# Kernel tuning notes

Hardware: AMD Instinct MI355X
Metric: run time of the kernel (lower is better)

The kernel has to match this reference:

```python
import jax, jax.numpy as jnp
import numpy as np

B, S, D, H = 8, 2048, 1024, 64


def setup_inputs() -> dict:
    key = jax.random.key(0)
    ks = jax.random.split(key, 9)
    s = 0.02
    return {
        "x": jax.random.normal(ks[0], (B, S, D), jnp.float32),
        "Wq": jax.random.normal(ks[1], (H, D), jnp.float32) * s,
        "bq": jnp.zeros((H,), jnp.float32),
        "Wk": jax.random.normal(ks[2], (H, D), jnp.float32) * s,
        "bk": jnp.zeros((H,), jnp.float32),
        "Wv": jax.random.normal(ks[3], (H, D), jnp.float32) * s,
        "bv": jnp.zeros((H,), jnp.float32),
        "Wo": jax.random.normal(ks[4], (H, H), jnp.float32) * s,
        "bo": jnp.zeros((H,), jnp.float32),
    }


def reference(x, Wq, bq, Wk, bk, Wv, bv, Wo, bo):
    # Linear layers: y = x @ W.T + b (torch nn.Linear convention)
    q = jnp.einsum("bsd,hd->bsh", x, Wq) + bq  # [B,S,H]
    k = jnp.einsum("bsd,hd->bsh", x, Wk) + bk
    v = jnp.einsum("bsd,hd->bsh", x, Wv) + bv
    scale = jnp.float32(H) ** 0.5
    scores = jnp.einsum("bsh,bth->bst", q, k) / scale  # [B,S,S]
    causal = jnp.tril(jnp.ones((S, S), bool))
    scores = jnp.where(causal, scores, -jnp.inf)
    attn = jax.nn.softmax(scores, axis=-1)
    out = jnp.einsum("bst,bth->bsh", attn, v)  # [B,S,H]
    out = jnp.einsum("bsh,gh->bsg", out, Wo) + bo  # output proj [H,H]
    return out
```

## Files before the change

### kernel.cpp

```cpp
#include <hip/hip_runtime.h>
#include <hip/hip_bf16.h>

#define NB 8
#define NS 2048
#define ND 1024
#define NH 64
#define NM (NB*NS)

typedef __attribute__((ext_vector_type(8))) short short8;
typedef __attribute__((ext_vector_type(4))) short short4v;
typedef __attribute__((ext_vector_type(4))) float f32x4;
typedef __attribute__((ext_vector_type(4))) float f4;
typedef __attribute__((ext_vector_type(2))) unsigned int uint2v;

#define QSCALE (0.125f * 1.44269504088896340736f)

__device__ __forceinline__ unsigned short f2bf(float f) {
    union { __hip_bfloat16 h; unsigned short u; } cv;
    cv.h = __float2bfloat16(f);
    return cv.u;
}

__device__ __forceinline__ void barrier_nd() {
    asm volatile("s_waitcnt lgkmcnt(0)" ::: "memory");
    __builtin_amdgcn_s_barrier();
    asm volatile("" ::: "memory");
}

__global__ __launch_bounds__(256) void convw_kernel(
    const float* __restrict__ Wq, const float* __restrict__ bq,
    const float* __restrict__ Wk, const float* __restrict__ bk,
    const float* __restrict__ Wv, const float* __restrict__ bv,
    const float* __restrict__ Wo,
    unsigned short* __restrict__ Wb, unsigned short* __restrict__ Wob,
    float* __restrict__ biasb)
{
    const int row = blockIdx.x;
    const int t = threadIdx.x;
    if (row < 192) {
        const float* W = row < 64 ? Wq : (row < 128 ? Wk : Wv);
        const float sc = row < 64 ? QSCALE : 1.0f;
        f4 v = *(const f4*)&W[(size_t)(row & 63) * ND + t * 4];
        short4v o;
#pragma unroll
        for (int j = 0; j < 4; ++j) o[j] = (short)f2bf(v[j] * sc);
        *(short4v*)&Wb[(size_t)row * ND + t * 4] = o;
        if (row == 0 && t < 192) {
            const float* bsrc = t < 64 ? bq : (t < 128 ? bk : bv);
            biasb[t] = bsrc[t & 63] * (t < 64 ? QSCALE : 1.0f);
        }
    } else if (t < 16) {
        f4 v = *(const f4*)&Wo[(size_t)(row - 192) * 64 + t * 4];
        short4v o;
#pragma unroll
        for (int j = 0; j < 4; ++j) o[j] = (short)f2bf(v[j]);
        *(short4v*)&Wob[(size_t)(row - 192) * 64 + t * 4] = o;
    }
}

__global__ __launch_bounds__(512, 2) void qkv_kernel(
    const float* __restrict__ x, const unsigned short* __restrict__ Wb,
    const float* __restrict__ biasb,
    unsigned short* __restrict__ q, unsigned short* __restrict__ k,
    unsigned short* __restrict__ vT)
{
    __shared__ unsigned short As[2][64 * 64];
    __shared__ unsigned short Bs[2][192 * 64];

    const int t = threadIdx.x;
    const int lane = t & 63, g = lane >> 4, li = lane & 15;
    const int w = t >> 6, rg = w >> 2, cg = w & 3;
    const int m0 = blockIdx.x * 64;
    const int arow = t >> 3, ach = t & 7;

    f32x4 acc[2][3];
#pragma unroll
    for (int a = 0; a < 2; ++a)
#pragma unroll
        for (int nf = 0; nf < 3; ++nf) acc[a][nf] = (f32x4)0.f;

    f4 xa[3][2]; short8 wr[3][3];

#define QKV_LOAD(KS, SL)                                                          \
    {                                                                             \
        const float* p_ = &x[(size_t)(m0 + arow) * ND + (KS) * 64 + ach * 8];     \
        xa[SL][0] = *(const f4*)p_; xa[SL][1] = *(const f4*)(p_ + 4);             \
        wr[SL][0] = *(const short8*)&Wb[(size_t)(t >> 3) * ND + (KS) * 64 + (t & 7) * 8];                  \
        wr[SL][1] = *(const short8*)&Wb[(size_t)((t + 512) >> 3) * ND + (KS) * 64 + ((t + 512) & 7) * 8];  \
        wr[SL][2] = *(const short8*)&Wb[(size_t)((t + 1024) >> 3) * ND + (KS) * 64 + ((t + 1024) & 7) * 8];\
    }

#define QKV_COMMIT(SL, BUF)                                                       \
    {                                                                             \
        short8 av_;                                                               \
        for (int j_ = 0; j_ < 4; ++j_) {                                          \
            av_[j_] = (short)f2bf(xa[SL][0][j_]);                                 \
            av_[j_ + 4] = (short)f2bf(xa[SL][1][j_]);                             \
        }                                                                         \
        *(short8*)&As[BUF][arow * 64 + ((ach ^ (arow & 7)) << 3)] = av_;          \
        int r0_ = t >> 3, c0_ = t & 7;                                            \
        *(short8*)&Bs[BUF][r0_ * 64 + ((c0_ ^ (r0_ & 7)) << 3)] = wr[SL][0];      \
        int r1_ = (t + 512) >> 3, c1_ = (t + 512) & 7;                            \
        *(short8*)&Bs[BUF][r1_ * 64 + ((c1_ ^ (r1_ & 7)) << 3)] = wr[SL][1];      \
        int r2_ = (t + 1024) >> 3, c2_ = (t + 1024) & 7;                          \
        *(short8*)&Bs[BUF][r2_ * 64 + ((c2_ ^ (r2_ & 7)) << 3)] = wr[SL][2];      \
    }

    QKV_LOAD(0, 0);
    QKV_LOAD(1, 1);
    QKV_LOAD(2, 2);
    QKV_COMMIT(0, 0);
    barrier_nd();

#pragma unroll
    for (int ks = 0; ks < 16; ++ks) {
        const int cur = ks & 1;
        if (ks < 13) QKV_LOAD(ks + 3, (ks + 3) % 3);
#pragma unroll
        for (int h = 0; h < 2; ++h) {
            short8 af0 = *(const short8*)&As[cur][(rg * 32 + 0 + li) * 64 + (((g + 4 * h) ^ (li & 7)) << 3)];
            short8 af1 = *(const short8*)&As[cur][(rg * 32 + 16 + li) * 64 + (((g + 4 * h) ^ (li & 7)) << 3)];
#pragma unroll
            for (int nf = 0; nf < 3; ++nf) {
                short8 bf = *(const short8*)&Bs[cur][(cg * 48 + nf * 16 + li) * 64 + (((g + 4 * h) ^ (li & 7)) << 3)];
                acc[0][nf] = __builtin_amdgcn_mfma_f32_16x16x32_bf16(af0, bf, acc[0][nf], 0, 0, 0);
                acc[1][nf] = __builtin_amdgcn_mfma_f32_16x16x32_bf16(af1, bf, acc[1][nf], 0, 0, 0);
            }
        }
        if (ks < 15) QKV_COMMIT((ks + 1) % 3, cur ^ 1);
        barrier_nd();
    }

#pragma unroll
    for (int nf = 0; nf < 3; ++nf) {
        const int col = cg * 48 + nf * 16 + li;
        const float bias = biasb[col];
#pragma unroll
        for (int a = 0; a < 2; ++a) {
            const int row0 = m0 + rg * 32 + a * 16 + 4 * g;
            if (col < 64) {
#pragma unroll
                for (int i = 0; i < 4; ++i)
                    q[(size_t)(row0 + i) * NH + col] = f2bf(acc[a][nf][i] + bias);
            } else if (col < 128) {
#pragma unroll
                for (int i = 0; i < 4; ++i)
                    k[(size_t)(row0 + i) * NH + (col - 64)] = f2bf(acc[a][nf][i] + bias);
            } else {
                short4v pk;
#pragma unroll
                for (int i = 0; i < 4; ++i) pk[i] = (short)f2bf(acc[a][nf][i] + bias);
                const int bb = row0 >> 11, s = row0 & 2047;
                *(short4v*)&vT[(size_t)(bb * NH + (col - 128)) * NS + s] = pk;
            }
        }
    }
}

__global__ __launch_bounds__(256, 2) void attn_kernel(
    const unsigned short* __restrict__ q, const unsigned short* __restrict__ k,
    const unsigned short* __restrict__ vT,
    float* __restrict__ Opart, float* __restrict__ lpart,
    int ctLog, int MAXC)
{
    __shared__ unsigned short Ks[2][64 * 64];
    __shared__ unsigned short Vs[2][64 * 64];
    __shared__ unsigned short Ps[4][16 * 64];

    const int t = threadIdx.x;
    const int w = t >> 6, lane = t & 63, g = lane >> 4, li = lane & 15;
    const int b = blockIdx.x & 7;
    const int pid = blockIdx.x >> 3;
    const int CT = 1 << ctLog;

    int qt = 0, c = 0;
    {
        int acc = 0;
        for (int u = 31; u >= 0; --u) {
            int nch = (u + CT) >> ctLog;
            if (pid < acc + nch) { qt = u; c = pid - acc; break; }
            acc += nch;
        }
    }
    const int t0 = c * CT;
    const int rem = qt + 1 - t0;
    const int tcount = rem < CT ? rem : CT;

    const size_t qkbase = (size_t)b * NS * NH;
    const int qrow = qt * 64 + w * 16 + li;
    const short8 qa0 = *(const short8*)&q[qkbase + (size_t)qrow * NH + g * 8];
    const short8 qa1 = *(const short8*)&q[qkbase + (size_t)qrow * NH + 32 + g * 8];

    float l_i = 0.f;
    f32x4 oacc[4];
#pragma unroll
    for (int i = 0; i < 4; ++i) oacc[i] = (f32x4)0.f;

    const int srow = t >> 3, sch = t & 7;
    short8 kreg0, kreg1, vreg0, vreg1;

    {
        const int kv0 = t0 * 64;
        kreg0 = *(const short8*)&k[qkbase + (size_t)(kv0 + srow) * NH + sch * 8];
        kreg1 = *(const short8*)&k[qkbase + (size_t)(kv0 + srow + 32) * NH + sch * 8];
        vreg0 = *(const short8*)&vT[(size_t)(b * NH + srow) * NS + kv0 + sch * 8];
        vreg1 = *(const short8*)&vT[(size_t)(b * NH + srow + 32) * NS + kv0 + sch * 8];
        *(short8*)&Ks[0][srow * 64 + ((sch ^ (srow & 7)) << 3)] = kreg0;
        *(short8*)&Ks[0][(srow + 32) * 64 + ((sch ^ (srow & 7)) << 3)] = kreg1;
        *(short8*)&Vs[0][srow * 64 + ((sch ^ (srow & 7)) << 3)] = vreg0;
        *(short8*)&Vs[0][(srow + 32) * 64 + ((sch ^ (srow & 7)) << 3)] = vreg1;
    }
    barrier_nd();

    for (int tt = 0; tt < tcount; ++tt) {
        const int cur = tt & 1;
        const int kv0 = (t0 + tt) * 64;
        if (tt + 1 < tcount) {
            const int nv0 = kv0 + 64;
            kreg0 = *(const short8*)&k[qkbase + (size_t)(nv0 + srow) * NH + sch * 8];
            kreg1 = *(const short8*)&k[qkbase + (size_t)(nv0 + srow + 32) * NH + sch * 8];
            vreg0 = *(const short8*)&vT[(size_t)(b * NH + srow) * NS + nv0 + sch * 8];
            vreg1 = *(const short8*)&vT[(size_t)(b * NH + srow + 32) * NS + nv0 + sch * 8];
        }
        f32x4 s[4];
#pragma unroll
        for (int c4 = 0; c4 < 4; ++c4) {
            s[c4] = (f32x4)0.f;
            const int krow = 16 * c4 + li;
            short8 kf0 = *(const short8*)&Ks[cur][krow * 64 + ((g ^ (li & 7)) << 3)];
            s[c4] = __builtin_amdgcn_mfma_f32_16x16x32_bf16(kf0, qa0, s[c4], 0, 0, 0);
            short8 kf1 = *(const short8*)&Ks[cur][krow * 64 + (((g + 4) ^ (li & 7)) << 3)];
            s[c4] = __builtin_amdgcn_mfma_f32_16x16x32_bf16(kf1, qa1, s[c4], 0, 0, 0);
        }
        if (kv0 == qt * 64) {
#pragma unroll
            for (int c4 = 0; c4 < 4; ++c4)
#pragma unroll
                for (int i = 0; i < 4; ++i)
                    if (16 * c4 + 4 * g + i > w * 16 + li) s[c4][i] = -1e30f;
        }
#pragma unroll
        for (int c4 = 0; c4 < 4; ++c4) {
#pragma unroll
            for (int i = 0; i < 4; ++i) {
                s[c4][i] = exp2f(fminf(s[c4][i], 80.f));
                l_i += s[c4][i];
            }
        }
#pragma unroll
        for (int c4 = 0; c4 < 4; ++c4) {
            unsigned lo = (unsigned)f2bf(s[c4][0]) | ((unsigned)f2bf(s[c4][1]) << 16);
            unsigned hi = (unsigned)f2bf(s[c4][2]) | ((unsigned)f2bf(s[c4][3]) << 16);
            uint2v pv; pv.x = lo; pv.y = hi;
            const int chunk = 2 * c4 + (g >> 1);
            *(uint2v*)&Ps[w][li * 64 + ((chunk ^ (li & 7)) << 3) + 4 * (g & 1)] = pv;
        }
        short8 pf0 = *(const short8*)&Ps[w][li * 64 + ((g ^ (li & 7)) << 3)];
        short8 pf1 = *(const short8*)&Ps[w][li * 64 + (((g + 4) ^ (li & 7)) << 3)];
#pragma unroll
        for (int nf = 0; nf < 4; ++nf) {
            const int vrow = nf * 16 + li;
            short8 vf0 = *(const short8*)&Vs[cur][vrow * 64 + ((g ^ (li & 7)) << 3)];
            short8 vf1 = *(const short8*)&Vs[cur][vrow * 64 + (((g + 4) ^ (li & 7)) << 3)];
            oacc[nf] = __builtin_amdgcn_mfma_f32_16x16x32_bf16(vf0, pf0, oacc[nf], 0, 0, 0);
            oacc[nf] = __builtin_amdgcn_mfma_f32_16x16x32_bf16(vf1, pf1, oacc[nf], 0, 0, 0);
        }
        if (tt + 1 < tcount) {
            *(short8*)&Ks[cur ^ 1][srow * 64 + ((sch ^ (srow & 7)) << 3)] = kreg0;
            *(short8*)&Ks[cur ^ 1][(srow + 32) * 64 + ((sch ^ (srow & 7)) << 3)] = kreg1;
            *(short8*)&Vs[cur ^ 1][srow * 64 + ((sch ^ (srow & 7)) << 3)] = vreg0;
            *(short8*)&Vs[cur ^ 1][(srow + 32) * 64 + ((sch ^ (srow & 7)) << 3)] = vreg1;
        }
        barrier_nd();
    }

    l_i += __shfl_xor(l_i, 16);
    l_i += __shfl_xor(l_i, 32);

    const size_t slot = (size_t)((b * 32 + qt) * MAXC + c);
    float* Op = Opart + slot * 4096;
#pragma unroll
    for (int nf = 0; nf < 4; ++nf)
#pragma unroll
        for (int i = 0; i < 4; ++i)
            Op[(w * 16 + li) * 64 + nf * 16 + 4 * g + i] = oacc[nf][i];
    if (g == 0)
        lpart[slot * 64 + w * 16 + li] = l_i;
}

__global__ __launch_bounds__(256, 2) void combine_kernel(
    const float* __restrict__ Opart, const float* __restrict__ lpart,
    const unsigned short* __restrict__ Wob, const float* __restrict__ bo,
    float* __restrict__ out, int ctLog, int MAXC)
{
    __shared__ unsigned short Osm[64 * 64];
    __shared__ float Linv[64];

    const int t = threadIdx.x;
    const int b = blockIdx.x & 7, qt = blockIdx.x >> 3;
    const int CT = 1 << ctLog;
    const int nch = (qt + CT) >> ctLog;
    const size_t base_slot = (size_t)(b * 32 + qt) * MAXC;

    if (t < 64) {
        float L = 0.f;
        for (int cc = 0; cc < nch; ++cc)
            L += lpart[(base_slot + cc) * 64 + t];
        Linv[t] = 1.f / L;
    }

    const int r = t >> 2, c0 = (t & 3) * 16;
    f4 a0 = (f4)0.f, a1 = (f4)0.f, a2 = (f4)0.f, a3 = (f4)0.f;
    for (int cc = 0; cc < nch; ++cc) {
        const float* P = Opart + (base_slot + cc) * 4096 + r * 64 + c0;
        a0 += *(const f4*)P; a1 += *(const f4*)(P + 4);
        a2 += *(const f4*)(P + 8); a3 += *(const f4*)(P + 12);
    }
    __syncthreads();
    {
        const float sc = Linv[r];
        short8 o0, o1;
#pragma unroll
        for (int j = 0; j < 4; ++j) {
            o0[j] = (short)f2bf(a0[j] * sc); o0[j + 4] = (short)f2bf(a1[j] * sc);
            o1[j] = (short)f2bf(a2[j] * sc); o1[j + 4] = (short)f2bf(a3[j] * sc);
        }
        const int ch0 = (t & 3) * 2;
        *(short8*)&Osm[r * 64 + ((ch0 ^ (r & 7)) << 3)] = o0;
        *(short8*)&Osm[r * 64 + (((ch0 + 1) ^ (r & 7)) << 3)] = o1;
    }
    __syncthreads();

    const int w = t >> 6, lane = t & 63, g = lane >> 4, li = lane & 15;
    f32x4 acc[4];
#pragma unroll
    for (int nf = 0; nf < 4; ++nf) acc[nf] = (f32x4)0.f;
#pragma unroll
    for (int s = 0; s < 2; ++s) {
        const int rr = w * 16 + li;
        short8 af = *(const short8*)&Osm[rr * 64 + (((g + 4 * s) ^ (rr & 7)) << 3)];
#pragma unroll
        for (int nf = 0; nf < 4; ++nf) {
            short8 bf = *(const short8*)&Wob[(size_t)(nf * 16 + li) * 64 + s * 32 + g * 8];
            acc[nf] = __builtin_amdgcn_mfma_f32_16x16x32_bf16(af, bf, acc[nf], 0, 0, 0);
        }
    }
#pragma unroll
    for (int nf = 0; nf < 4; ++nf) {
        const float bias = bo[nf * 16 + li];
#pragma unroll
        for (int i = 0; i < 4; ++i) {
            const size_t row = (size_t)b * NS + qt * 64 + w * 16 + 4 * g + i;
            out[row * 64 + nf * 16 + li] = acc[nf][i] + bias;
        }
    }
}

extern "C" void kernel_launch(void* const* d_in, const int* in_sizes, int n_in,
                              void* d_out, int out_size, void* d_ws, size_t ws_size,
                              hipStream_t stream)
{
    const float* x  = (const float*)d_in[0];
    const float* Wq = (const float*)d_in[1];
    const float* bq = (const float*)d_in[2];
    const float* Wk = (const float*)d_in[3];
    const float* bk = (const float*)d_in[4];
    const float* Wv = (const float*)d_in[5];
    const float* bv = (const float*)d_in[6];
    const float* Wo = (const float*)d_in[7];
    const float* bo = (const float*)d_in[8];
    float* out = (float*)d_out;

    size_t off = 0;
    auto alloc = [&](size_t bytes) {
        char* p = (char*)d_ws + off;
        off += (bytes + 255) & ~(size_t)255;
        return (void*)p;
    };
    unsigned short* qb  = (unsigned short*)alloc((size_t)NM * NH * 2);
    unsigned short* kb  = (unsigned short*)alloc((size_t)NM * NH * 2);
    unsigned short* vtb = (unsigned short*)alloc((size_t)NM * NH * 2);
    unsigned short* Wb  = (unsigned short*)alloc((size_t)192 * ND * 2);
    unsigned short* Wob = (unsigned short*)alloc((size_t)64 * 64 * 2);
    float* biasb = (float*)alloc(192 * 4);
    const size_t base = off;

    int ctLog = 5, MAXC = 1;
    const int cands[3] = {3, 4, 5};
    for (int ci = 0; ci < 3; ++ci) {
        const int cl = cands[ci];
        const int mc = (31 >> cl) + 1;
        const size_t nslot = (size_t)256 * mc;
        const size_t need = base + nslot * (4096 + 64) * 4 + 8192;
        if (need <= ws_size) { ctLog = cl; MAXC = mc; break; }
    }
    const size_t NSLOT = (size_t)256 * MAXC;
    float* Opart = (float*)alloc(NSLOT * 4096 * 4);
    float* lpart = (float*)alloc(NSLOT * 64 * 4);

    const int CT = 1 << ctLog;
    int NCperB = 0;
    for (int qt = 0; qt < 32; ++qt) NCperB += (qt + CT) >> ctLog;

    convw_kernel<<<256, 256, 0, stream>>>(Wq, bq, Wk, bk, Wv, bv, Wo, Wb, Wob, biasb);
    qkv_kernel<<<NM / 64, 512, 0, stream>>>(x, Wb, biasb, qb, kb, vtb);
    attn_kernel<<<8 * NCperB, 256, 0, stream>>>(qb, kb, vtb, Opart, lpart, ctLog, MAXC);
    combine_kernel<<<256, 256, 0, stream>>>(Opart, lpart, Wob, bo, out, ctLog, MAXC);
}
```

Before: 47.41 us.

## Split QKV projection GEMM along K with a separate reduction kernel

Splits the QKV projection across two K halves, doubling the block count so every CU can host two blocks. Each half writes fp32 partial sums to workspace. A new reduce kernel adds the partials, applies bias and converts to bf16 for q, k and transposed v. This trades extra partial-sum memory traffic and an additional launch for higher occupancy and better latency hiding in the x-streaming GEMM.

```diff
diff --git a/kernel.cpp b/kernel.cpp
--- a/kernel.cpp
+++ b/kernel.cpp
@@ -58,11 +58,9 @@
     }
 }
 
-__global__ __launch_bounds__(512, 2) void qkv_kernel(
+__global__ __launch_bounds__(512, 2) void qkv_main_kernel(
     const float* __restrict__ x, const unsigned short* __restrict__ Wb,
-    const float* __restrict__ biasb,
-    unsigned short* __restrict__ q, unsigned short* __restrict__ k,
-    unsigned short* __restrict__ vT)
+    float* __restrict__ PartQK, float* __restrict__ PartV)
 {
     __shared__ unsigned short As[2][64 * 64];
     __shared__ unsigned short Bs[2][192 * 64];
@@ -70,7 +68,9 @@
     const int t = threadIdx.x;
     const int lane = t & 63, g = lane >> 4, li = lane & 15;
     const int w = t >> 6, rg = w >> 2, cg = w & 3;
-    const int m0 = blockIdx.x * 64;
+    const int m0 = (blockIdx.x >> 1) * 64;
+    const int kh = blockIdx.x & 1;
+    const int KS0 = kh * 8;
     const int arow = t >> 3, ach = t & 7;
 
     f32x4 acc[2][3];
@@ -83,11 +83,11 @@
 
 #define QKV_LOAD(KS, SL)                                                          \
     {                                                                             \
-        const float* p_ = &x[(size_t)(m0 + arow) * ND + (KS) * 64 + ach * 8];     \
+        const float* p_ = &x[(size_t)(m0 + arow) * ND + (KS0 + (KS)) * 64 + ach * 8]; \
         xa[SL][0] = *(const f4*)p_; xa[SL][1] = *(const f4*)(p_ + 4);             \
-        wr[SL][0] = *(const short8*)&Wb[(size_t)(t >> 3) * ND + (KS) * 64 + (t & 7) * 8];                  \
-        wr[SL][1] = *(const short8*)&Wb[(size_t)((t + 512) >> 3) * ND + (KS) * 64 + ((t + 512) & 7) * 8];  \
-        wr[SL][2] = *(const short8*)&Wb[(size_t)((t + 1024) >> 3) * ND + (KS) * 64 + ((t + 1024) & 7) * 8];\
+        wr[SL][0] = *(const short8*)&Wb[(size_t)(t >> 3) * ND + (KS0 + (KS)) * 64 + (t & 7) * 8];                  \
+        wr[SL][1] = *(const short8*)&Wb[(size_t)((t + 512) >> 3) * ND + (KS0 + (KS)) * 64 + ((t + 512) & 7) * 8];  \
+        wr[SL][2] = *(const short8*)&Wb[(size_t)((t + 1024) >> 3) * ND + (KS0 + (KS)) * 64 + ((t + 1024) & 7) * 8];\
     }
 
 #define QKV_COMMIT(SL, BUF)                                                       \
@@ -113,9 +113,9 @@
     barrier_nd();
 
 #pragma unroll
-    for (int ks = 0; ks < 16; ++ks) {
+    for (int ks = 0; ks < 8; ++ks) {
         const int cur = ks & 1;
-        if (ks < 13) QKV_LOAD(ks + 3, (ks + 3) % 3);
+        if (ks < 5) QKV_LOAD(ks + 3, (ks + 3) % 3);
 #pragma unroll
         for (int h = 0; h < 2; ++h) {
             short8 af0 = *(const short8*)&As[cur][(rg * 32 + 0 + li) * 64 + (((g + 4 * h) ^ (li & 7)) << 3)];
@@ -127,33 +127,63 @@
                 acc[1][nf] = __builtin_amdgcn_mfma_f32_16x16x32_bf16(af1, bf, acc[1][nf], 0, 0, 0);
             }
         }
-        if (ks < 15) QKV_COMMIT((ks + 1) % 3, cur ^ 1);
+        if (ks < 7) QKV_COMMIT((ks + 1) % 3, cur ^ 1);
         barrier_nd();
     }
 
+    float* pqk = PartQK + (size_t)kh * NM * 128;
+    float* pv  = PartV  + (size_t)kh * NM * 64;
 #pragma unroll
     for (int nf = 0; nf < 3; ++nf) {
         const int col = cg * 48 + nf * 16 + li;
-        const float bias = biasb[col];
 #pragma unroll
         for (int a = 0; a < 2; ++a) {
             const int row0 = m0 + rg * 32 + a * 16 + 4 * g;
-            if (col < 64) {
+            if (col < 128) {
 #pragma unroll
                 for (int i = 0; i < 4; ++i)
-                    q[(size_t)(row0 + i) * NH + col] = f2bf(acc[a][nf][i] + bias);
-            } else if (col < 128) {
-#pragma unroll
-                for (int i = 0; i < 4; ++i)
-                    k[(size_t)(row0 + i) * NH + (col - 64)] = f2bf(acc[a][nf][i] + bias);
+                    pqk[(size_t)(row0 + i) * 128 + col] = acc[a][nf][i];
             } else {
-                short4v pk;
-#pragma unroll
-                for (int i = 0; i < 4; ++i) pk[i] = (short)f2bf(acc[a][nf][i] + bias);
+                const int hh = col - 128;
                 const int bb = row0 >> 11, s = row0 & 2047;
-                *(short4v*)&vT[(size_t)(bb * NH + (col - 128)) * NS + s] = pk;
+                f4 vv;
+#pragma unroll
+                for (int i = 0; i < 4; ++i) vv[i] = acc[a][nf][i];
+                *(f4*)&pv[(size_t)(bb * 64 + hh) * NS + s] = vv;
             }
         }
+    }
+}
+
+__global__ __launch_bounds__(256) void qkv_reduce_kernel(
+    const float* __restrict__ PartQK, const float* __restrict__ PartV,
+    const float* __restrict__ biasb,
+    unsigned short* __restrict__ q, unsigned short* __restrict__ k,
+    unsigned short* __restrict__ vT)
+{
+    const int t = threadIdx.x;
+    if (blockIdx.x < 2048) {
+        const int gid = blockIdx.x * 256 + t;
+        const int row = gid >> 5, c4 = (gid & 31) * 4;
+        f4 v = *(const f4*)&PartQK[(size_t)row * 128 + c4];
+        f4 v2 = *(const f4*)&PartQK[(size_t)(NM + row) * 128 + c4];
+        short4v o;
+#pragma unroll
+        for (int j = 0; j < 4; ++j)
+            o[j] = (short)f2bf(v[j] + v2[j] + biasb[c4 + j]);
+        if (c4 < 64) *(short4v*)&q[(size_t)row * NH + c4] = o;
+        else         *(short4v*)&k[(size_t)row * NH + (c4 - 64)] = o;
+    } else {
+        const int gid = (blockIdx.x - 2048) * 256 + t;
+        const int bh = gid >> 9, s4 = (gid & 511) * 4;
+        f4 v = *(const f4*)&PartV[(size_t)bh * NS + s4];
+        f4 v2 = *(const f4*)&PartV[(size_t)(NM * 64 / NS + bh) * NS + s4];
+        const float bias = biasb[128 + (bh & 63)];
+        short4v o;
+#pragma unroll
+        for (int j = 0; j < 4; ++j)
+            o[j] = (short)f2bf(v[j] + v2[j] + bias);
+        *(short4v*)&vT[(size_t)bh * NS + s4] = o;
     }
 }
 
@@ -383,6 +413,8 @@
     unsigned short* Wb  = (unsigned short*)alloc((size_t)192 * ND * 2);
     unsigned short* Wob = (unsigned short*)alloc((size_t)64 * 64 * 2);
     float* biasb = (float*)alloc(192 * 4);
+    float* PartQK = (float*)alloc((size_t)2 * NM * 128 * 4);
+    float* PartV  = (float*)alloc((size_t)2 * NM * 64 * 4);
     const size_t base = off;
 
     int ctLog = 5, MAXC = 1;
@@ -403,7 +435,8 @@
     for (int qt = 0; qt < 32; ++qt) NCperB += (qt + CT) >> ctLog;
 
     convw_kernel<<<256, 256, 0, stream>>>(Wq, bq, Wk, bk, Wv, bv, Wo, Wb, Wob, biasb);
-    qkv_kernel<<<NM / 64, 512, 0, stream>>>(x, Wb, biasb, qb, kb, vtb);
+    qkv_main_kernel<<<2 * (NM / 64), 512, 0, stream>>>(x, Wb, PartQK, PartV);
+    qkv_reduce_kernel<<<3072, 256, 0, stream>>>(PartQK, PartV, biasb, qb, kb, vtb);
     attn_kernel<<<8 * NCperB, 256, 0, stream>>>(qb, kb, vtb, Opart, lpart, ctLog, MAXC);
     combine_kernel<<<256, 256, 0, stream>>>(Opart, lpart, Wob, bo, out, ctLog, MAXC);
 }
```

Measured after the change: 57.05 us. +20.3%, slower.

## Enlarge attention query tile to 128 rows, sharing each K/V tile across two subtiles

Applied to the files above, without the earlier changes.

Each attention block now handles 128 query rows (32 per wave, as two 16-row subtiles) instead of 64. Every K/V tile staged in shared memory therefore feeds twice as many MFMAs, which halves K/V global traffic per query row. Waves whose rows lie entirely before a KV tile skip its compute, and the partial-output layout, combine kernel and split-chunk selection (now allowing CT=4) are adapted to match. In exchange the kernel needs more registers and LDS and launches fewer blocks, and causal masking leaves more imbalance within each block.

```diff
diff --git a/kernel.cpp b/kernel.cpp
--- a/kernel.cpp
+++ b/kernel.cpp
@@ -165,7 +165,7 @@
 {
     __shared__ unsigned short Ks[2][64 * 64];
     __shared__ unsigned short Vs[2][64 * 64];
-    __shared__ unsigned short Ps[4][16 * 64];
+    __shared__ unsigned short Ps[4][32 * 64];
 
     const int t = threadIdx.x;
     const int w = t >> 6, lane = t & 63, g = lane >> 4, li = lane & 15;
@@ -173,28 +173,35 @@
     const int pid = blockIdx.x >> 3;
     const int CT = 1 << ctLog;
 
-    int qt = 0, c = 0;
+    int qb = 0, c = 0;
     {
         int acc = 0;
-        for (int u = 31; u >= 0; --u) {
-            int nch = (u + CT) >> ctLog;
-            if (pid < acc + nch) { qt = u; c = pid - acc; break; }
+        for (int u = 15; u >= 0; --u) {
+            const int nch = (2 * u + 2 + CT - 1) >> ctLog;
+            if (pid < acc + nch) { qb = u; c = pid - acc; break; }
             acc += nch;
         }
     }
     const int t0 = c * CT;
-    const int rem = qt + 1 - t0;
+    const int ntt = 2 * qb + 2;
+    const int rem = ntt - t0;
     const int tcount = rem < CT ? rem : CT;
 
     const size_t qkbase = (size_t)b * NS * NH;
-    const int qrow = qt * 64 + w * 16 + li;
-    const short8 qa0 = *(const short8*)&q[qkbase + (size_t)qrow * NH + g * 8];
-    const short8 qa1 = *(const short8*)&q[qkbase + (size_t)qrow * NH + 32 + g * 8];
-
-    float l_i = 0.f;
-    f32x4 oacc[4];
-#pragma unroll
-    for (int i = 0; i < 4; ++i) oacc[i] = (f32x4)0.f;
+    const int q0w = qb * 128 + w * 32;
+    short8 qa[2][2];
+#pragma unroll
+    for (int qs = 0; qs < 2; ++qs)
+#pragma unroll
+        for (int h = 0; h < 2; ++h)
+            qa[qs][h] = *(const short8*)&q[qkbase + (size_t)(q0w + qs * 16 + li) * NH + h * 32 + g * 8];
+
+    float l_i[2] = {0.f, 0.f};
+    f32x4 oacc[2][4];
+#pragma unroll
+    for (int qs = 0; qs < 2; ++qs)
+#pragma unroll
+        for (int i = 0; i < 4; ++i) oacc[qs][i] = (f32x4)0.f;
 
     const int srow = t >> 3, sch = t & 7;
     short8 kreg0, kreg1, vreg0, vreg1;
@@ -222,48 +229,63 @@
             vreg0 = *(const short8*)&vT[(size_t)(b * NH + srow) * NS + nv0 + sch * 8];
             vreg1 = *(const short8*)&vT[(size_t)(b * NH + srow + 32) * NS + nv0 + sch * 8];
         }
-        f32x4 s[4];
-#pragma unroll
-        for (int c4 = 0; c4 < 4; ++c4) {
-            s[c4] = (f32x4)0.f;
-            const int krow = 16 * c4 + li;
-            short8 kf0 = *(const short8*)&Ks[cur][krow * 64 + ((g ^ (li & 7)) << 3)];
-            s[c4] = __builtin_amdgcn_mfma_f32_16x16x32_bf16(kf0, qa0, s[c4], 0, 0, 0);
-            short8 kf1 = *(const short8*)&Ks[cur][krow * 64 + (((g + 4) ^ (li & 7)) << 3)];
-            s[c4] = __builtin_amdgcn_mfma_f32_16x16x32_bf16(kf1, qa1, s[c4], 0, 0, 0);
-        }
-        if (kv0 == qt * 64) {
-#pragma unroll
-            for (int c4 = 0; c4 < 4; ++c4)
-#pragma unroll
-                for (int i = 0; i < 4; ++i)
-                    if (16 * c4 + 4 * g + i > w * 16 + li) s[c4][i] = -1e30f;
-        }
-#pragma unroll
-        for (int c4 = 0; c4 < 4; ++c4) {
-#pragma unroll
-            for (int i = 0; i < 4; ++i) {
-                s[c4][i] = exp2f(fminf(s[c4][i], 80.f));
-                l_i += s[c4][i];
-            }
-        }
-#pragma unroll
-        for (int c4 = 0; c4 < 4; ++c4) {
-            unsigned lo = (unsigned)f2bf(s[c4][0]) | ((unsigned)f2bf(s[c4][1]) << 16);
-            unsigned hi = (unsigned)f2bf(s[c4][2]) | ((unsigned)f2bf(s[c4][3]) << 16);
-            uint2v pv; pv.x = lo; pv.y = hi;
-            const int chunk = 2 * c4 + (g >> 1);
-            *(uint2v*)&Ps[w][li * 64 + ((chunk ^ (li & 7)) << 3) + 4 * (g & 1)] = pv;
-        }
-        short8 pf0 = *(const short8*)&Ps[w][li * 64 + ((g ^ (li & 7)) << 3)];
-        short8 pf1 = *(const short8*)&Ps[w][li * 64 + (((g + 4) ^ (li & 7)) << 3)];
-#pragma unroll
-        for (int nf = 0; nf < 4; ++nf) {
-            const int vrow = nf * 16 + li;
-            short8 vf0 = *(const short8*)&Vs[cur][vrow * 64 + ((g ^ (li & 7)) << 3)];
-            short8 vf1 = *(const short8*)&Vs[cur][vrow * 64 + (((g + 4) ^ (li & 7)) << 3)];
-            oacc[nf] = __builtin_amdgcn_mfma_f32_16x16x32_bf16(vf0, pf0, oacc[nf], 0, 0, 0);
-            oacc[nf] = __builtin_amdgcn_mfma_f32_16x16x32_bf16(vf1, pf1, oacc[nf], 0, 0, 0);
+        if (kv0 <= q0w + 31) {
+            f32x4 s[2][4];
+#pragma unroll
+            for (int c4 = 0; c4 < 4; ++c4) {
+                s[0][c4] = (f32x4)0.f; s[1][c4] = (f32x4)0.f;
+                const int krow = 16 * c4 + li;
+                short8 kf0 = *(const short8*)&Ks[cur][krow * 64 + ((g ^ (li & 7)) << 3)];
+                short8 kf1 = *(const short8*)&Ks[cur][krow * 64 + (((g + 4) ^ (li & 7)) << 3)];
+                s[0][c4] = __builtin_amdgcn_mfma_f32_16x16x32_bf16(kf0, qa[0][0], s[0][c4], 0, 0, 0);
+                s[0][c4] = __builtin_amdgcn_mfma_f32_16x16x32_bf16(kf1, qa[0][1], s[0][c4], 0, 0, 0);
+                s[1][c4] = __builtin_amdgcn_mfma_f32_16x16x32_bf16(kf0, qa[1][0], s[1][c4], 0, 0, 0);
+                s[1][c4] = __builtin_amdgcn_mfma_f32_16x16x32_bf16(kf1, qa[1][1], s[1][c4], 0, 0, 0);
+            }
+            if (kv0 + 63 > q0w) {
+#pragma unroll
+                for (int qs = 0; qs < 2; ++qs)
+#pragma unroll
+                    for (int c4 = 0; c4 < 4; ++c4)
+#pragma unroll
+                        for (int i = 0; i < 4; ++i)
+                            if (kv0 + 16 * c4 + 4 * g + i > q0w + qs * 16 + li)
+                                s[qs][c4][i] = -1e30f;
+            }
+#pragma unroll
+            for (int qs = 0; qs < 2; ++qs) {
+                const int prow = qs * 16 + li;
+#pragma unroll
+                for (int c4 = 0; c4 < 4; ++c4) {
+#pragma unroll
+                    for (int i = 0; i < 4; ++i) {
+                        s[qs][c4][i] = exp2f(fminf(s[qs][c4][i], 80.f));
+                        l_i[qs] += s[qs][c4][i];
+                    }
+                    unsigned lo = (unsigned)f2bf(s[qs][c4][0]) | ((unsigned)f2bf(s[qs][c4][1]) << 16);
+                    unsigned hi = (unsigned)f2bf(s[qs][c4][2]) | ((unsigned)f2bf(s[qs][c4][3]) << 16);
+                    uint2v pv; pv.x = lo; pv.y = hi;
+                    const int chunk = 2 * c4 + (g >> 1);
+                    *(uint2v*)&Ps[w][prow * 64 + ((chunk ^ (li & 7)) << 3) + 4 * (g & 1)] = pv;
+                }
+            }
+            short8 pf[2][2];
+#pragma unroll
+            for (int qs = 0; qs < 2; ++qs) {
+                const int prow = qs * 16 + li;
+                pf[qs][0] = *(const short8*)&Ps[w][prow * 64 + ((g ^ (li & 7)) << 3)];
+                pf[qs][1] = *(const short8*)&Ps[w][prow * 64 + (((g + 4) ^ (li & 7)) << 3)];
+            }
+#pragma unroll
+            for (int nf = 0; nf < 4; ++nf) {
+                const int vrow = nf * 16 + li;
+                short8 vf0 = *(const short8*)&Vs[cur][vrow * 64 + ((g ^ (li & 7)) << 3)];
+                short8 vf1 = *(const short8*)&Vs[cur][vrow * 64 + (((g + 4) ^ (li & 7)) << 3)];
+                oacc[0][nf] = __builtin_amdgcn_mfma_f32_16x16x32_bf16(vf0, pf[0][0], oacc[0][nf], 0, 0, 0);
+                oacc[0][nf] = __builtin_amdgcn_mfma_f32_16x16x32_bf16(vf1, pf[0][1], oacc[0][nf], 0, 0, 0);
+                oacc[1][nf] = __builtin_amdgcn_mfma_f32_16x16x32_bf16(vf0, pf[1][0], oacc[1][nf], 0, 0, 0);
+                oacc[1][nf] = __builtin_amdgcn_mfma_f32_16x16x32_bf16(vf1, pf[1][1], oacc[1][nf], 0, 0, 0);
+            }
         }
         if (tt + 1 < tcount) {
             *(short8*)&Ks[cur ^ 1][srow * 64 + ((sch ^ (srow & 7)) << 3)] = kreg0;
@@ -274,18 +296,25 @@
         barrier_nd();
     }
 
-    l_i += __shfl_xor(l_i, 16);
-    l_i += __shfl_xor(l_i, 32);
-
-    const size_t slot = (size_t)((b * 32 + qt) * MAXC + c);
-    float* Op = Opart + slot * 4096;
-#pragma unroll
-    for (int nf = 0; nf < 4; ++nf)
-#pragma unroll
-        for (int i = 0; i < 4; ++i)
-            Op[(w * 16 + li) * 64 + nf * 16 + 4 * g + i] = oacc[nf][i];
-    if (g == 0)
-        lpart[slot * 64 + w * 16 + li] = l_i;
+#pragma unroll
+    for (int qs = 0; qs < 2; ++qs) {
+        l_i[qs] += __shfl_xor(l_i[qs], 16);
+        l_i[qs] += __shfl_xor(l_i[qs], 32);
+    }
+
+    const size_t slot = (size_t)((b * 16 + qb) * MAXC + c);
+    float* Op = Opart + slot * 8192;
+#pragma unroll
+    for (int qs = 0; qs < 2; ++qs)
+#pragma unroll
+        for (int nf = 0; nf < 4; ++nf)
+#pragma unroll
+            for (int i = 0; i < 4; ++i)
+                Op[(w * 32 + qs * 16 + li) * 64 + nf * 16 + 4 * g + i] = oacc[qs][nf][i];
+    if (g == 0) {
+        lpart[slot * 128 + w * 32 + li]      = l_i[0];
+        lpart[slot * 128 + w * 32 + 16 + li] = l_i[1];
+    }
 }
 
 __global__ __launch_bounds__(256, 2) void combine_kernel(
@@ -297,22 +326,23 @@
     __shared__ float Linv[64];
 
     const int t = threadIdx.x;
-    const int b = blockIdx.x & 7, qt = blockIdx.x >> 3;
+    const int b = blockIdx.x & 7, qb = (blockIdx.x >> 3) & 15, half = blockIdx.x >> 7;
+    const int r0 = half * 64;
     const int CT = 1 << ctLog;
-    const int nch = (qt + CT) >> ctLog;
-    const size_t base_slot = (size_t)(b * 32 + qt) * MAXC;
+    const int nch = (2 * qb + 2 + CT - 1) >> ctLog;
+    const size_t base_slot = (size_t)(b * 16 + qb) * MAXC;
 
     if (t < 64) {
         float L = 0.f;
         for (int cc = 0; cc < nch; ++cc)
-            L += lpart[(base_slot + cc) * 64 + t];
+            L += lpart[(base_slot + cc) * 128 + r0 + t];
         Linv[t] = 1.f / L;
     }
 
     const int r = t >> 2, c0 = (t & 3) * 16;
     f4 a0 = (f4)0.f, a1 = (f4)0.f, a2 = (f4)0.f, a3 = (f4)0.f;
     for (int cc = 0; cc < nch; ++cc) {
-        const float* P = Opart + (base_slot + cc) * 4096 + r * 64 + c0;
+        const float* P = Opart + (base_slot + cc) * 8192 + (r0 + r) * 64 + c0;
         a0 += *(const f4*)P; a1 += *(const f4*)(P + 4);
         a2 += *(const f4*)(P + 8); a3 += *(const f4*)(P + 12);
     }
@@ -350,7 +380,7 @@
         const float bias = bo[nf * 16 + li];
 #pragma unroll
         for (int i = 0; i < 4; ++i) {
-            const size_t row = (size_t)b * NS + qt * 64 + w * 16 + 4 * g + i;
+            const size_t row = (size_t)b * NS + qb * 128 + r0 + w * 16 + 4 * g + i;
             out[row * 64 + nf * 16 + li] = acc[nf][i] + bias;
         }
     }
@@ -386,21 +416,21 @@
     const size_t base = off;
 
     int ctLog = 5, MAXC = 1;
-    const int cands[3] = {3, 4, 5};
-    for (int ci = 0; ci < 3; ++ci) {
+    const int cands[4] = {2, 3, 4, 5};
+    for (int ci = 0; ci < 4; ++ci) {
         const int cl = cands[ci];
-        const int mc = (31 >> cl) + 1;
-        const size_t nslot = (size_t)256 * mc;
-        const size_t need = base + nslot * (4096 + 64) * 4 + 8192;
+        const int mc = 32 >> cl;
+        const size_t nslot = (size_t)128 * mc;
+        const size_t need = base + nslot * (8192 + 128) * 4 + 8192;
         if (need <= ws_size) { ctLog = cl; MAXC = mc; break; }
     }
-    const size_t NSLOT = (size_t)256 * MAXC;
-    float* Opart = (float*)alloc(NSLOT * 4096 * 4);
-    float* lpart = (float*)alloc(NSLOT * 64 * 4);
+    const size_t NSLOT = (size_t)128 * MAXC;
+    float* Opart = (float*)alloc(NSLOT * 8192 * 4);
+    float* lpart = (float*)alloc(NSLOT * 128 * 4);
 
     const int CT = 1 << ctLog;
     int NCperB = 0;
-    for (int qt = 0; qt < 32; ++qt) NCperB += (qt + CT) >> ctLog;
+    for (int u = 0; u < 16; ++u) NCperB += (2 * u + 2 + CT - 1) >> ctLog;
 
     convw_kernel<<<256, 256, 0, stream>>>(Wq, bq, Wk, bk, Wv, bv, Wo, Wb, Wob, biasb);
     qkv_kernel<<<NM / 64, 512, 0, stream>>>(x, Wb, biasb, qb, kb, vtb);
```

Result: slower. 51.06 us (+7.7%).

## Stage x in 256-wide K chunks with separate weight pipeline in QKV GEMM

Applied to the files above, without the earlier changes.

The QKV projection kernel now loads x in 256-column chunks: each thread reads 128 contiguous bytes as eight float4 loads and converts them to bf16 into a 4x larger double-buffered LDS tile. Weight tiles keep their own 64-wide double buffer, with one-step lookahead instead of the old three-deep register ring. The goal is wider, more coalesced global reads of x and fewer x commit points. In exchange, LDS use per block grows to about 112 KB, which may not fit two 512-thread blocks per CU. The x prefetch also needs many more registers.

```diff
diff --git a/kernel.cpp b/kernel.cpp
--- a/kernel.cpp
+++ b/kernel.cpp
@@ -64,14 +64,14 @@
     unsigned short* __restrict__ q, unsigned short* __restrict__ k,
     unsigned short* __restrict__ vT)
 {
-    __shared__ unsigned short As[2][64 * 64];
+    __shared__ unsigned short As4[2][64 * 256];
     __shared__ unsigned short Bs[2][192 * 64];
 
     const int t = threadIdx.x;
     const int lane = t & 63, g = lane >> 4, li = lane & 15;
     const int w = t >> 6, rg = w >> 2, cg = w & 3;
     const int m0 = blockIdx.x * 64;
-    const int arow = t >> 3, ach = t & 7;
+    const int arow = t >> 3, seg = t & 7;
 
     f32x4 acc[2][3];
 #pragma unroll
@@ -79,25 +79,40 @@
 #pragma unroll
         for (int nf = 0; nf < 3; ++nf) acc[a][nf] = (f32x4)0.f;
 
-    f4 xa[3][2]; short8 wr[3][3];
-
-#define QKV_LOAD(KS, SL)                                                          \
+    f4 xa[2][8];
+    short8 wr[2][3];
+
+#define XLOAD4(KO, SL)                                                            \
     {                                                                             \
-        const float* p_ = &x[(size_t)(m0 + arow) * ND + (KS) * 64 + ach * 8];     \
-        xa[SL][0] = *(const f4*)p_; xa[SL][1] = *(const f4*)(p_ + 4);             \
+        const float* p_ = &x[(size_t)(m0 + arow) * ND + (KO) * 256 + seg * 32];   \
+        _Pragma("unroll")                                                         \
+        for (int j_ = 0; j_ < 8; ++j_) xa[SL][j_] = *(const f4*)(p_ + j_ * 4);    \
+    }
+
+#define XCOMMIT4(SL, BUF)                                                         \
+    {                                                                             \
+        _Pragma("unroll")                                                         \
+        for (int m_ = 0; m_ < 4; ++m_) {                                          \
+            short8 av_;                                                           \
+            for (int j_ = 0; j_ < 4; ++j_) {                                      \
+                av_[j_]     = (short)f2bf(xa[SL][2 * m_][j_]);                    \
+                av_[j_ + 4] = (short)f2bf(xa[SL][2 * m_ + 1][j_]);                \
+            }                                                                     \
+            const int gi_ = (seg & 1) * 4 + m_;                                   \
+            *(short8*)&As4[BUF][arow * 256 + (seg >> 1) * 64 +                    \
+                                ((gi_ ^ (arow & 7)) << 3)] = av_;                 \
+        }                                                                         \
+    }
+
+#define WLOAD(KS, SL)                                                             \
+    {                                                                             \
         wr[SL][0] = *(const short8*)&Wb[(size_t)(t >> 3) * ND + (KS) * 64 + (t & 7) * 8];                  \
         wr[SL][1] = *(const short8*)&Wb[(size_t)((t + 512) >> 3) * ND + (KS) * 64 + ((t + 512) & 7) * 8];  \
         wr[SL][2] = *(const short8*)&Wb[(size_t)((t + 1024) >> 3) * ND + (KS) * 64 + ((t + 1024) & 7) * 8];\
     }
 
-#define QKV_COMMIT(SL, BUF)                                                       \
+#define WCOMMIT(SL, BUF)                                                          \
     {                                                                             \
-        short8 av_;                                                               \
-        for (int j_ = 0; j_ < 4; ++j_) {                                          \
-            av_[j_] = (short)f2bf(xa[SL][0][j_]);                                 \
-            av_[j_ + 4] = (short)f2bf(xa[SL][1][j_]);                             \
-        }                                                                         \
-        *(short8*)&As[BUF][arow * 64 + ((ach ^ (arow & 7)) << 3)] = av_;          \
         int r0_ = t >> 3, c0_ = t & 7;                                            \
         *(short8*)&Bs[BUF][r0_ * 64 + ((c0_ ^ (r0_ & 7)) << 3)] = wr[SL][0];      \
         int r1_ = (t + 512) >> 3, c1_ = (t + 512) & 7;                            \
@@ -106,28 +121,37 @@
         *(short8*)&Bs[BUF][r2_ * 64 + ((c2_ ^ (r2_ & 7)) << 3)] = wr[SL][2];      \
     }
 
-    QKV_LOAD(0, 0);
-    QKV_LOAD(1, 1);
-    QKV_LOAD(2, 2);
-    QKV_COMMIT(0, 0);
+    XLOAD4(0, 0);
+    XLOAD4(1, 1);
+    WLOAD(0, 0);
+    XCOMMIT4(0, 0);
+    WCOMMIT(0, 0);
     barrier_nd();
 
 #pragma unroll
-    for (int ks = 0; ks < 16; ++ks) {
-        const int cur = ks & 1;
-        if (ks < 13) QKV_LOAD(ks + 3, (ks + 3) % 3);
-#pragma unroll
-        for (int h = 0; h < 2; ++h) {
-            short8 af0 = *(const short8*)&As[cur][(rg * 32 + 0 + li) * 64 + (((g + 4 * h) ^ (li & 7)) << 3)];
-            short8 af1 = *(const short8*)&As[cur][(rg * 32 + 16 + li) * 64 + (((g + 4 * h) ^ (li & 7)) << 3)];
-#pragma unroll
-            for (int nf = 0; nf < 3; ++nf) {
-                short8 bf = *(const short8*)&Bs[cur][(cg * 48 + nf * 16 + li) * 64 + (((g + 4 * h) ^ (li & 7)) << 3)];
-                acc[0][nf] = __builtin_amdgcn_mfma_f32_16x16x32_bf16(af0, bf, acc[0][nf], 0, 0, 0);
-                acc[1][nf] = __builtin_amdgcn_mfma_f32_16x16x32_bf16(af1, bf, acc[1][nf], 0, 0, 0);
+    for (int ko = 0; ko < 4; ++ko) {
+        const int abuf = ko & 1;
+        if (ko < 2) XLOAD4(ko + 2, abuf);
+#pragma unroll
+        for (int kk = 0; kk < 4; ++kk) {
+            const int ks = ko * 4 + kk;
+            const int wbuf = ks & 1;
+            if (ks < 15) WLOAD(ks + 1, wbuf ^ 1);
+#pragma unroll
+            for (int h = 0; h < 2; ++h) {
+                short8 af0 = *(const short8*)&As4[abuf][(rg * 32 + 0 + li) * 256 + kk * 64 + (((g + 4 * h) ^ (li & 7)) << 3)];
+                short8 af1 = *(const short8*)&As4[abuf][(rg * 32 + 16 + li) * 256 + kk * 64 + (((g + 4 * h) ^ (li & 7)) << 3)];
+#pragma unroll
+                for (int nf = 0; nf < 3; ++nf) {
+                    short8 bf = *(const short8*)&Bs[wbuf][(cg * 48 + nf * 16 + li) * 64 + (((g + 4 * h) ^ (li & 7)) << 3)];
+                    acc[0][nf] = __builtin_amdgcn_mfma_f32_16x16x32_bf16(af0, bf, acc[0][nf], 0, 0, 0);
+                    acc[1][nf] = __builtin_amdgcn_mfma_f32_16x16x32_bf16(af1, bf, acc[1][nf], 0, 0, 0);
+                }
             }
-        }
-        if (ks < 15) QKV_COMMIT((ks + 1) % 3, cur ^ 1);
+            if (ks < 15) WCOMMIT(wbuf ^ 1, wbuf ^ 1);
+            if (kk < 3) barrier_nd();
+        }
+        if (ko < 3) XCOMMIT4((ko + 1) & 1, (ko + 1) & 1);
         barrier_nd();
     }
 
```

Measured after the change: 56.68 us. 19.5% more time.
